# Kernel tuning notes

Hardware: AMD Instinct MI355X
Metric: run time of the kernel (lower is better)

The kernel has to match this reference:

```python
import jax, jax.numpy as jnp
import numpy as np

N, T, D = 2, 8192, 1024          # batch, seq (== maxlen), d_model
G, H, DQ, DV = 1, 16, 64, 64     # gqa groups, heads, d_queries, d_values
S = 16                           # infinite_attention_n_segments
L = T // S                       # segment length
EPS = 1e-05


def setup_inputs() -> dict:
    key = jax.random.key(0)
    ks = jax.random.split(key, 6)
    s = 0.02
    return {
        "x": jax.random.normal(ks[0], (N, T, D), jnp.float32),
        "ln_g": jnp.ones((D,), jnp.float32),
        "ln_b": jnp.zeros((D,), jnp.float32),
        "Wq": jax.random.normal(ks[1], (D, G * H * DQ), jnp.float32) * s,
        "bq": jnp.zeros((G * H * DQ,), jnp.float32),
        "Wk": jax.random.normal(ks[2], (D, H * DQ), jnp.float32) * s,
        "bk": jnp.zeros((H * DQ,), jnp.float32),
        "Wv": jax.random.normal(ks[3], (D, H * DV), jnp.float32) * s,
        "bv": jnp.zeros((H * DV,), jnp.float32),
        "Wo": jax.random.normal(ks[4], (H * DV, D), jnp.float32) * s,
        "bo": jnp.zeros((D,), jnp.float32),
        "beta": jnp.ones((1,), jnp.float32),
    }


def _layernorm(x, g, b):
    mu = jnp.mean(x, axis=-1, keepdims=True)
    var = jnp.mean(jnp.square(x - mu), axis=-1, keepdims=True)
    return (x - mu) * jax.lax.rsqrt(var + EPS) * g + b


def _apply_rotary(t):
    # t: [..., seq, d]; lucidrains rotary-embedding-torch convention (interleaved pairs)
    d, seq = t.shape[-1], t.shape[-2]
    inv = 1.0 / (10000.0 ** (jnp.arange(0, d, 2, dtype=jnp.float32) / d))
    freqs = jnp.arange(seq, dtype=jnp.float32)[:, None] * inv[None, :]  # (seq, d/2)
    freqs = jnp.repeat(freqs, 2, axis=-1)                               # (seq, d)
    cos, sin = jnp.cos(freqs), jnp.sin(freqs)
    x1, x2 = t[..., 0::2], t[..., 1::2]
    rot = jnp.stack([-x2, x1], axis=-1).reshape(t.shape)
    return t * cos + rot * sin


def reference(x, ln_g, ln_b, Wq, bq, Wk, bk, Wv, bv, Wo, bo, beta):
    xn = _layernorm(x, ln_g, ln_b)  # self-attn: same norm for q/k/v
    q = (xn @ Wq + bq).reshape(N, T, G, H, DQ).transpose(0, 2, 3, 1, 4)  # (N,G,H,T,DQ)
    k = (xn @ Wk + bk).reshape(N, T, H, DQ).transpose(0, 2, 1, 3)        # (N,H,T,DQ)
    v = (xn @ Wv + bv).reshape(N, T, H, DV).transpose(0, 2, 1, 3)        # (N,H,T,DV)

    q = _apply_rotary(q)
    k = _apply_rotary(k)

    # segment: (S, N, G, H, L, d) / (S, N, H, L, d)
    qs = jnp.moveaxis(q.reshape(N, G, H, S, L, DQ), 3, 0)
    ks = jnp.moveaxis(k.reshape(N, H, S, L, DQ), 2, 0)
    vs = jnp.moveaxis(v.reshape(N, H, S, L, DV), 2, 0)

    causal = jnp.tril(jnp.ones((L, L), bool))
    scale = 1.0 / (DQ ** 0.5)
    g_beta = jax.nn.sigmoid(beta)[0]

    def step(carry, seg):
        memory, z = carry                     # (N,H,DQ,DV), (N,H,DQ,DQ)
        q_i, k_i, v_i = seg                   # (N,G,H,L,DQ), (N,H,L,DQ), (N,H,L,DV)
        sq = jax.nn.elu(q_i) + 1.0
        sk = jax.nn.elu(k_i) + 1.0
        A_mem = jnp.einsum('nghld,nhde->nghle', sq, memory) / (
            jnp.einsum('nghld,nhde->nghle', sq, z) + 1e-6)
        # note: einsum sums over g (faithful to source); scores (N,H,L,L)
        attn = jnp.einsum('nghld,nhmd->nhlm', q_i, k_i) * scale
        attn = jnp.where(causal, attn, -jnp.inf)
        attn = jax.nn.softmax(attn, axis=-1)
        local = jnp.einsum('nhlm,nhmd->nhld', attn, v_i)
        out = g_beta * A_mem + (1.0 - g_beta) * local[:, None]  # (N,G,H,L,DV)
        memory = memory + jnp.einsum('nhld,nhle->nhde', sk, v_i)          # linear update
        z = z + jnp.sum(sk, axis=-2, keepdims=True)  # (N,H,1,DQ) broadcast (source quirk)
        return (memory, z), out

    mem0 = jnp.zeros((N, H, DQ, DV), jnp.float32)
    z0 = jnp.zeros((N, H, DQ, DQ), jnp.float32)
    _, ys = jax.lax.scan(step, (mem0, z0), (qs, ks, vs))  # ys: (S,N,G,H,L,DV)

    # torch concat along head dim (segment-major) then view(N, t, -1)
    seqs = jnp.transpose(ys, (1, 2, 0, 3, 4, 5)).reshape(N, T, G * H * DV)
    return seqs @ Wo + bo
```

## Files before the change

kernel.cpp:

```cpp
#include <hip/hip_runtime.h>
#include <hip/hip_bf16.h>
#include <math.h>

#define NT 16384
#define DD 1024
#define QKVN 3072

typedef unsigned short u16;
typedef _Float16 half8 __attribute__((ext_vector_type(8)));
typedef float f32x4 __attribute__((ext_vector_type(4)));

#define DEV static __device__ __forceinline__

DEV float h2f(u16 u) { _Float16 h; __builtin_memcpy(&h, &u, 2); return (float)h; }
DEV u16 f2h(float f) { _Float16 h = (_Float16)f; u16 u; __builtin_memcpy(&u, &h, 2); return u; }
DEV f32x4 mfma16(half8 a, half8 b, f32x4 c) {
  return __builtin_amdgcn_mfma_f32_16x16x32_f16(a, b, c, 0, 0, 0);
}
DEV half8 ld8(const u16* p) { return *(const half8*)p; }
DEV float elu1(float x) { return x > 0.f ? x + 1.f : __expf(x); }
DEV void gll16(const void* g, void* l) {
  __builtin_amdgcn_global_load_lds((const __attribute__((address_space(1))) void*)g,
                                   (__attribute__((address_space(3))) void*)l, 16, 0, 0);
}

__global__ __launch_bounds__(256) void prep_w(const float* __restrict__ Wq,
    const float* __restrict__ Wk, const float* __restrict__ Wv,
    const float* __restrict__ Wo, u16* __restrict__ WqkvT, u16* __restrict__ WoT) {
  __shared__ float tile[64][65];
  const int mat = blockIdx.z;
  const float* src = mat == 0 ? Wq : mat == 1 ? Wk : mat == 2 ? Wv : Wo;
  const int d0 = blockIdx.x * 64, c0 = blockIdx.y * 64;
  const int t = threadIdx.x;
#pragma unroll
  for (int i = 0; i < 16; ++i) {
    int rl = (t >> 6) + i * 4;
    tile[rl][t & 63] = src[(size_t)(d0 + rl) * DD + c0 + (t & 63)];
  }
  __syncthreads();
  u16* dst = mat < 3 ? WqkvT + (size_t)mat * DD * DD : WoT;
#pragma unroll
  for (int i = 0; i < 16; ++i) {
    int cl = (t >> 6) + i * 4;
    dst[(size_t)(c0 + cl) * DD + d0 + (t & 63)] = f2h(tile[t & 63][cl]);
  }
}

__global__ void pack_bias(const float* __restrict__ bq, const float* __restrict__ bk,
                          const float* __restrict__ bv, float* __restrict__ bqkv) {
  int i = blockIdx.x * 256 + threadIdx.x;
  if (i < 1024) bqkv[i] = bq[i];
  else if (i < 2048) bqkv[i] = bk[i - 1024];
  else if (i < 3072) bqkv[i] = bv[i - 2048];
}

__global__ __launch_bounds__(256) void rope_table(float* __restrict__ tab) {
  int idx = blockIdx.x * 256 + threadIdx.x;
  int tp = idx >> 5, i = idx & 31;
  double inv = exp(-(double)i * (log(10000.0) / 32.0));
  double ang = (double)tp * inv;
  tab[idx * 2]     = (float)cos(ang);
  tab[idx * 2 + 1] = (float)sin(ang);
}

__global__ __launch_bounds__(256) void lnorm(const float* __restrict__ x,
    const float* __restrict__ g, const float* __restrict__ b, u16* __restrict__ xn) {
  const int row = blockIdx.x, t = threadIdx.x;
  float4 v = ((const float4*)x)[(size_t)row * 256 + t];
  float s = v.x + v.y + v.z + v.w;
  float sq = v.x * v.x + v.y * v.y + v.z * v.z + v.w * v.w;
  for (int o = 32; o; o >>= 1) { s += __shfl_down(s, o); sq += __shfl_down(sq, o); }
  __shared__ float ps[4], pq[4];
  const int w = t >> 6, lane = t & 63;
  if (lane == 0) { ps[w] = s; pq[w] = sq; }
  __syncthreads();
  s = ps[0] + ps[1] + ps[2] + ps[3];
  sq = pq[0] + pq[1] + pq[2] + pq[3];
  float mu = s * (1.f / 1024.f);
  float var = sq * (1.f / 1024.f) - mu * mu;
  float rs = rsqrtf(var + 1e-5f);
  float4 gg = ((const float4*)g)[t], bb = ((const float4*)b)[t];
  float o0 = (v.x - mu) * rs * gg.x + bb.x;
  float o1 = (v.y - mu) * rs * gg.y + bb.y;
  float o2 = (v.z - mu) * rs * gg.z + bb.z;
  float o3 = (v.w - mu) * rs * gg.w + bb.w;
  uint2 u2;
  u2.x = (unsigned)f2h(o0) | ((unsigned)f2h(o1) << 16);
  u2.y = (unsigned)f2h(o2) | ((unsigned)f2h(o3) << 16);
  *(uint2*)&xn[(size_t)row * 1024 + t * 4] = u2;
}

template <bool OUT_F16>
__global__ __launch_bounds__(256) void gemm_bt(const u16* __restrict__ A,
    const u16* __restrict__ BT, const float* __restrict__ bias,
    void* __restrict__ C, int M, int N, int K) {
  __shared__ u16 As[128 * 32];
  __shared__ u16 Bs[128 * 32];
  const int t = threadIdx.x;
  const int lane = t & 63, w = t >> 6;
  const int wr = w >> 1, wc = w & 1;
  const int m0 = blockIdx.x * 128, n0 = blockIdx.y * 128;
  const int srow = w * 16 + (lane >> 2);
  const int schunk = lane & 3;
  int aoff[4], boff[4];
#pragma unroll
  for (int i = 0; i < 4; ++i) {
    int ra = wr * 64 + i * 16 + (lane & 15);
    aoff[i] = ra * 32 + (((lane >> 4) ^ ((ra >> 1) & 3)) * 8);
    int rb = wc * 64 + i * 16 + (lane & 15);
    boff[i] = rb * 32 + (((lane >> 4) ^ ((rb >> 1) & 3)) * 8);
  }
  f32x4 acc[4][4] = {};
  for (int k0 = 0; k0 < K; k0 += 32) {
#pragma unroll
    for (int i = 0; i < 2; ++i) {
      int row = srow + i * 64;
      int gc = (schunk ^ ((row >> 1) & 3)) * 8;
      gll16(&A[(size_t)(m0 + row) * K + k0 + gc], &As[(w * 16 + i * 64) * 32]);
      gll16(&BT[(size_t)(n0 + row) * K + k0 + gc], &Bs[(w * 16 + i * 64) * 32]);
    }
    __syncthreads();
    half8 af[4], bfr[4];
#pragma unroll
    for (int i = 0; i < 4; ++i) {
      af[i]  = ld8(&As[aoff[i]]);
      bfr[i] = ld8(&Bs[boff[i]]);
    }
#pragma unroll
    for (int mi = 0; mi < 4; ++mi)
#pragma unroll
      for (int ni = 0; ni < 4; ++ni)
        acc[mi][ni] = mfma16(af[mi], bfr[ni], acc[mi][ni]);
    __syncthreads();
  }
  const int rg = lane >> 4, cl = lane & 15;
#pragma unroll
  for (int mi = 0; mi < 4; ++mi)
#pragma unroll
    for (int r = 0; r < 4; ++r) {
      size_t row = (size_t)(m0 + wr * 64 + mi * 16 + rg * 4 + r);
#pragma unroll
      for (int ni = 0; ni < 4; ++ni) {
        int col = n0 + wc * 64 + ni * 16 + cl;
        float v = acc[mi][ni][r] + bias[col];
        if (OUT_F16) ((u16*)C)[row * N + col] = f2h(v);
        else ((float*)C)[row * N + col] = v;
      }
    }
}

__global__ __launch_bounds__(256) void rope_apply(u16* __restrict__ qkv,
                                                  const float* __restrict__ tab) {
  const int row = blockIdx.x, t = threadIdx.x;
  const int c = t * 8;
  const int tp = row & 8191;
  const int d0 = c & 63;
  size_t off = (size_t)row * QKVN + c;
  union { uint4 v; u16 s[8]; } q;
  q.v = *(const uint4*)&qkv[off];
  float4 cs0 = *(const float4*)&tab[(tp * 32 + (d0 >> 1)) * 2];
  float4 cs1 = *(const float4*)&tab[(tp * 32 + (d0 >> 1)) * 2 + 4];
  float co[4] = {cs0.x, cs0.z, cs1.x, cs1.z};
  float si[4] = {cs0.y, cs0.w, cs1.y, cs1.w};
#pragma unroll
  for (int j = 0; j < 4; ++j) {
    float x0 = h2f(q.s[2 * j]), x1 = h2f(q.s[2 * j + 1]);
    q.s[2 * j]     = f2h(x0 * co[j] - x1 * si[j]);
    q.s[2 * j + 1] = f2h(x1 * co[j] + x0 * si[j]);
  }
  *(uint4*)&qkv[off] = q.v;
}

__global__ __launch_bounds__(256) void segstats(const u16* __restrict__ qkv,
    float* __restrict__ Mseg, float* __restrict__ Zseg) {
  __shared__ float skL[128][64];
  __shared__ float vL[128][64];
  const int b = blockIdx.x;
  const int seg = b & 15, h = (b >> 4) & 15, n = b >> 8;
  const int t = threadIdx.x;
  const int d = t >> 2, e0 = (t & 3) * 16;
  float acc[16] = {};
  float zacc = 0.f;
  const size_t base = (size_t)(n * 8192 + seg * 512) * QKVN;
  for (int ch = 0; ch < 4; ++ch) {
#pragma unroll
    for (int p = 0; p < 4; ++p) {
      int r = (t >> 3) + 32 * p;
      int cs = (t & 7) * 8;
      size_t ro = base + (size_t)(ch * 128 + r) * QKVN + h * 64 + cs;
      union { uint4 v; u16 s[8]; } kk, vv;
      kk.v = *(const uint4*)&qkv[ro + 1024];
      vv.v = *(const uint4*)&qkv[ro + 2048];
#pragma unroll
      for (int j = 0; j < 8; ++j) {
        skL[r][cs + j] = elu1(h2f(kk.s[j]));
        vL[r][cs + j] = h2f(vv.s[j]);
      }
    }
    __syncthreads();
    for (int l = 0; l < 128; ++l) {
      float s = skL[l][d];
      zacc += s;
      const float4* vr = (const float4*)&vL[l][e0];
      float4 a0 = vr[0], a1 = vr[1], a2 = vr[2], a3 = vr[3];
      acc[0] += s * a0.x;  acc[1] += s * a0.y;  acc[2] += s * a0.z;  acc[3] += s * a0.w;
      acc[4] += s * a1.x;  acc[5] += s * a1.y;  acc[6] += s * a1.z;  acc[7] += s * a1.w;
      acc[8] += s * a2.x;  acc[9] += s * a2.y;  acc[10] += s * a2.z; acc[11] += s * a2.w;
      acc[12] += s * a3.x; acc[13] += s * a3.y; acc[14] += s * a3.z; acc[15] += s * a3.w;
    }
    __syncthreads();
  }
  size_t mb = (size_t)b * 4096 + d * 64 + e0;
  float4 o0 = {acc[0], acc[1], acc[2], acc[3]};
  float4 o1 = {acc[4], acc[5], acc[6], acc[7]};
  float4 o2 = {acc[8], acc[9], acc[10], acc[11]};
  float4 o3 = {acc[12], acc[13], acc[14], acc[15]};
  *(float4*)&Mseg[mb] = o0; *(float4*)&Mseg[mb + 4] = o1;
  *(float4*)&Mseg[mb + 8] = o2; *(float4*)&Mseg[mb + 12] = o3;
  if ((t & 3) == 0) Zseg[(size_t)b * 64 + d] = zacc;
}

__global__ __launch_bounds__(256) void prefix_k(const float* __restrict__ Mseg,
    const float* __restrict__ Zseg, u16* __restrict__ MpT, float* __restrict__ Zpre) {
  const int nh = blockIdx.x;
  const int t = threadIdx.x;
  const int e = t >> 2, d0 = (t & 3) * 16;
  float acc[16] = {};
  for (int s = 0; s < 16; ++s) {
    size_t bb = (size_t)(nh * 16 + s) * 4096;
    union { uint4 v[2]; u16 hh[16]; } o;
#pragma unroll
    for (int j = 0; j < 16; ++j) o.hh[j] = f2h(acc[j]);
    *(uint4*)&MpT[bb + e * 64 + d0] = o.v[0];
    *(uint4*)&MpT[bb + e * 64 + d0 + 8] = o.v[1];
#pragma unroll
    for (int j = 0; j < 16; ++j) acc[j] += Mseg[bb + (size_t)(d0 + j) * 64 + e];
  }
  if (t < 16) {
    float4 zac = {0.f, 0.f, 0.f, 0.f};
    for (int s = 0; s < 16; ++s) {
      size_t idx = (size_t)(nh * 16 + s) * 64 + t * 4;
      *(float4*)&Zpre[idx] = zac;
      float4 z = *(const float4*)&Zseg[idx];
      zac.x += z.x; zac.y += z.y; zac.z += z.z; zac.w += z.w;
    }
  }
}

struct SmemA { u16 Ks[64][72]; u16 VTs[64][72]; u16 Ps[64][72]; };
struct SmemB { u16 sqH[64][72]; u16 MpTs[64][72]; float rowS[64]; };
union SmemU { SmemA a; SmemB b; };

__global__ __launch_bounds__(256, 3) void attn_seg(const u16* __restrict__ qkv,
    const u16* __restrict__ MpT, const float* __restrict__ Zpre,
    const float* __restrict__ beta, u16* __restrict__ ao) {
  __shared__ __align__(16) u16 Qs[64][72];
  __shared__ __align__(16) SmemU U;
  const int b = (blockIdx.x & 7) * 512 + (blockIdx.x >> 3);
  const int qt = b & 7, seg = (b >> 3) & 15, h = (b >> 7) & 15, n = b >> 11;
  const int t = threadIdx.x, lane = t & 63, w = t >> 6;

  const size_t qbase = (size_t)(n * 8192 + seg * 512 + qt * 64) * QKVN + h * 64;
#pragma unroll
  for (int p = 0; p < 2; ++p) {
    int r = p * 32 + (t >> 3), cs = (t & 7) * 8;
    *(uint4*)&Qs[r][cs] = *(const uint4*)&qkv[qbase + (size_t)r * QKVN + cs];
  }

  const int r0 = t >> 3;
  const int cs = (t & 7) * 8;
  const int vcol1 = (((w) ^ (t & 7)) << 3) | (r0 & 7);
  const int vcol2 = (((w + 4) ^ (t & 7)) << 3) | (r0 & 7);
  const size_t kbase = (size_t)(n * 8192 + seg * 512) * QKVN + h * 64 + cs;

  uint4 kk0, kk1, vv0, vv1;
  {
    size_t ro = kbase + (size_t)r0 * QKVN;
    kk0 = *(const uint4*)&qkv[ro + 1024];
    vv0 = *(const uint4*)&qkv[ro + 2048];
    kk1 = *(const uint4*)&qkv[ro + 32 * QKVN + 1024];
    vv1 = *(const uint4*)&qkv[ro + 32 * QKVN + 2048];
  }
  __syncthreads();
  half8 aq0 = ld8(&Qs[w * 16 + (lane & 15)][(lane >> 4) * 8]);
  half8 aq1 = ld8(&Qs[w * 16 + (lane & 15)][32 + (lane >> 4) * 8]);

  float mrow[4], lrow[4];
  f32x4 oacc[4] = {};
#pragma unroll
  for (int r = 0; r < 4; ++r) { mrow[r] = -INFINITY; lrow[r] = 0.f; }

  for (int mt = 0; mt <= qt; ++mt) {
    *(uint4*)&U.a.Ks[r0][cs] = kk0;
    *(uint4*)&U.a.Ks[r0 + 32][cs] = kk1;
    union { uint4 v; u16 s[8]; } u0, u1;
    u0.v = vv0; u1.v = vv1;
#pragma unroll
    for (int j = 0; j < 8; ++j) {
      U.a.VTs[cs + j][vcol1] = u0.s[j];
      U.a.VTs[cs + j][vcol2] = u1.s[j];
    }
    if (mt < qt) {
      size_t ro = kbase + (size_t)((mt + 1) * 64 + r0) * QKVN;
      kk0 = *(const uint4*)&qkv[ro + 1024];
      vv0 = *(const uint4*)&qkv[ro + 2048];
      kk1 = *(const uint4*)&qkv[ro + 32 * QKVN + 1024];
      vv1 = *(const uint4*)&qkv[ro + 32 * QKVN + 2048];
    }
    __syncthreads();

    f32x4 s[4] = {};
#pragma unroll
    for (int ni = 0; ni < 4; ++ni) {
      half8 b0 = ld8(&U.a.Ks[ni * 16 + (lane & 15)][(lane >> 4) * 8]);
      half8 b1 = ld8(&U.a.Ks[ni * 16 + (lane & 15)][32 + (lane >> 4) * 8]);
      s[ni] = mfma16(aq0, b0, s[ni]);
      s[ni] = mfma16(aq1, b1, s[ni]);
    }
    float pm[4];
#pragma unroll
    for (int r = 0; r < 4; ++r) {
      int ql = qt * 64 + w * 16 + (lane >> 4) * 4 + r;
      float mx = -INFINITY;
#pragma unroll
      for (int ni = 0; ni < 4; ++ni) {
        float v = s[ni][r] * 0.125f;
        if (mt == qt) { int ml = mt * 64 + ni * 16 + (lane & 15); if (ml > ql) v = -INFINITY; }
        s[ni][r] = v; mx = fmaxf(mx, v);
      }
      pm[r] = mx;
    }
#pragma unroll
    for (int o = 1; o < 16; o <<= 1)
#pragma unroll
      for (int r = 0; r < 4; ++r) pm[r] = fmaxf(pm[r], __shfl_xor(pm[r], o, 16));
    float fac[4], rs[4];
#pragma unroll
    for (int r = 0; r < 4; ++r) {
      float mn = fmaxf(mrow[r], pm[r]);
      fac[r] = __expf(mrow[r] - mn);
      mrow[r] = mn;
      float a = 0.f;
#pragma unroll
      for (int ni = 0; ni < 4; ++ni) { float p = __expf(s[ni][r] - mn); s[ni][r] = p; a += p; }
      rs[r] = a;
    }
#pragma unroll
    for (int o = 1; o < 16; o <<= 1)
#pragma unroll
      for (int r = 0; r < 4; ++r) rs[r] += __shfl_xor(rs[r], o, 16);
#pragma unroll
    for (int r = 0; r < 4; ++r) {
      lrow[r] = lrow[r] * fac[r] + rs[r];
#pragma unroll
      for (int ei = 0; ei < 4; ++ei) oacc[ei][r] *= fac[r];
    }
#pragma unroll
    for (int ni = 0; ni < 4; ++ni)
#pragma unroll
      for (int r = 0; r < 4; ++r)
        U.a.Ps[w * 16 + (lane >> 4) * 4 + r][ni * 16 + (lane & 15)] = f2h(s[ni][r]);
#pragma unroll
    for (int ks = 0; ks < 2; ++ks) {
      half8 ap = ld8(&U.a.Ps[w * 16 + (lane & 15)][ks * 32 + (lane >> 4) * 8]);
#pragma unroll
      for (int ei = 0; ei < 4; ++ei) {
        int erow = ei * 16 + (lane & 15);
        int ccol = (((ks * 4 + (lane >> 4)) ^ (ei * 2 + ((lane & 15) >> 3))) << 3);
        half8 bv = ld8(&U.a.VTs[erow][ccol]);
        oacc[ei] = mfma16(ap, bv, oacc[ei]);
      }
    }
    __syncthreads();
  }

  {
    const int q = t >> 2, c0 = (t & 3) * 16;
    union { uint2 v; u16 s[4]; } qa;
    float partial = 0.f;
    union { uint4 v; u16 hh[8]; } o;
#pragma unroll
    for (int half = 0; half < 2; ++half) {
#pragma unroll
      for (int jj = 0; jj < 2; ++jj) {
        qa.v = *(const uint2*)&Qs[q][c0 + half * 8 + jj * 4];
#pragma unroll
        for (int k4 = 0; k4 < 4; ++k4) {
          float sv = elu1(h2f(qa.s[k4]));
          partial += sv;
          o.hh[jj * 4 + k4] = f2h(sv);
        }
      }
      *(uint4*)&U.b.sqH[q][c0 + half * 8] = o.v;
    }
    partial += __shfl_xor(partial, 1);
    partial += __shfl_xor(partial, 2);
    if ((t & 3) == 0) U.b.rowS[q] = partial;
  }
  const size_t mpb = (size_t)((n * 16 + h) * 16 + seg) * 4096;
#pragma unroll
  for (int p = 0; p < 2; ++p) {
    int e = p * 32 + (t >> 3), c = (t & 7) * 8;
    *(uint4*)&U.b.MpTs[e][c] = *(const uint4*)&MpT[mpb + e * 64 + c];
  }
  __syncthreads();

  f32x4 num[4] = {};
#pragma unroll
  for (int ks = 0; ks < 2; ++ks) {
    half8 asq = ld8(&U.b.sqH[w * 16 + (lane & 15)][ks * 32 + (lane >> 4) * 8]);
#pragma unroll
    for (int ni = 0; ni < 4; ++ni) {
      half8 bmp = ld8(&U.b.MpTs[ni * 16 + (lane & 15)][ks * 32 + (lane >> 4) * 8]);
      num[ni] = mfma16(asq, bmp, num[ni]);
    }
  }

  const float gb = 1.f / (1.f + __expf(-beta[0]));
  const size_t zb = (size_t)((n * 16 + h) * 16 + seg) * 64;
  const int g = lane >> 4;
  float rsv[4];
#pragma unroll
  for (int r = 0; r < 4; ++r) rsv[r] = U.b.rowS[w * 16 + g * 4 + r];
  const size_t orow = ((size_t)(n * 8192 + seg * 512 + h * 32 + qt * 4 + w)) * 1024;
#pragma unroll
  for (int ni = 0; ni < 4; ++ni) {
    float z = Zpre[zb + ni * 16 + (lane & 15)];
#pragma unroll
    for (int r = 0; r < 4; ++r) {
      float am = num[ni][r] / (rsv[r] * z + 1e-6f);
      float loc = oacc[ni][r] / lrow[r];
      float val = gb * am + (1.f - gb) * loc;
      ao[orow + (size_t)(g * 4 + r) * 64 + ni * 16 + (lane & 15)] = f2h(val);
    }
  }
}

extern "C" void kernel_launch(void* const* d_in, const int* in_sizes, int n_in,
                              void* d_out, int out_size, void* d_ws, size_t ws_size,
                              hipStream_t stream) {
  const float* x    = (const float*)d_in[0];
  const float* ln_g = (const float*)d_in[1];
  const float* ln_b = (const float*)d_in[2];
  const float* Wq   = (const float*)d_in[3];
  const float* bq   = (const float*)d_in[4];
  const float* Wk   = (const float*)d_in[5];
  const float* bk   = (const float*)d_in[6];
  const float* Wv   = (const float*)d_in[7];
  const float* bv   = (const float*)d_in[8];
  const float* Wo   = (const float*)d_in[9];
  const float* bo   = (const float*)d_in[10];
  const float* beta = (const float*)d_in[11];
  float* out = (float*)d_out;

  char* w = (char*)d_ws;
  u16*   xn    = (u16*)(w + 0);
  u16*   qkv   = (u16*)(w + 33554432ull);
  u16*   WqkvT = (u16*)(w + 134217728ull);
  u16*   WoT   = (u16*)(w + 140509184ull);
  float* bqkv  = (float*)(w + 142606336ull);
  float* tab   = (float*)(w + 142618624ull);
  float* Mseg  = (float*)(w + 144715776ull);
  float* Zseg  = (float*)(w + 153104384ull);
  u16*   MpT   = (u16*)(w + 153235456ull);
  float* Zpre  = (float*)(w + 161624064ull);
  u16*   ao    = (u16*)(w + 161755136ull);

  prep_w<<<dim3(16, 16, 4), 256, 0, stream>>>(Wq, Wk, Wv, Wo, WqkvT, WoT);
  pack_bias<<<12, 256, 0, stream>>>(bq, bk, bv, bqkv);
  rope_table<<<1024, 256, 0, stream>>>(tab);
  lnorm<<<16384, 256, 0, stream>>>(x, ln_g, ln_b, xn);
  gemm_bt<true><<<dim3(128, 24), 256, 0, stream>>>(xn, WqkvT, bqkv, (void*)qkv, NT, QKVN, DD);
  rope_apply<<<16384, 256, 0, stream>>>(qkv, tab);
  segstats<<<512, 256, 0, stream>>>(qkv, Mseg, Zseg);
  prefix_k<<<32, 256, 0, stream>>>(Mseg, Zseg, MpT, Zpre);
  attn_seg<<<4096, 256, 0, stream>>>(qkv, MpT, Zpre, beta, ao);
  gemm_bt<false><<<dim3(128, 8), 256, 0, stream>>>(ao, WoT, bo, (void*)out, NT, DD, DD);
}
```

Measured before the change: 524.9 us.

## Use 256x256 double-buffered GEMM and transpose segment stats for coalesced prefix

Replaces the 128x128 single-buffered GEMM with a 256x256-tile, 512-thread kernel. The new kernel double-buffers K-chunks in 128KB of dynamic LDS, interleaves global-to-LDS staging with MFMA phases, raises wave priority during MFMA and swizzles block IDs for L2 locality. Segstats now transposes its memory stats through LDS so prefix_k reads contiguous float4 and spreads over 128 blocks instead of 32. The large LDS footprint limits occupancy, and the hand-written vmcnt waits must match the load counts exactly.

Result: faster. 489.7 us (-6.7%).

```diff
diff --git a/kernel.cpp b/kernel.cpp
--- a/kernel.cpp
+++ b/kernel.cpp
@@ -91,57 +91,125 @@
 }
 
 template <bool OUT_F16>
-__global__ __launch_bounds__(256) void gemm_bt(const u16* __restrict__ A,
+__global__ __launch_bounds__(512, 2) void gemm256(const u16* __restrict__ A,
     const u16* __restrict__ BT, const float* __restrict__ bias,
-    void* __restrict__ C, int M, int N, int K) {
-  __shared__ u16 As[128 * 32];
-  __shared__ u16 Bs[128 * 32];
-  const int t = threadIdx.x;
-  const int lane = t & 63, w = t >> 6;
-  const int wr = w >> 1, wc = w & 1;
-  const int m0 = blockIdx.x * 128, n0 = blockIdx.y * 128;
-  const int srow = w * 16 + (lane >> 2);
-  const int schunk = lane & 3;
-  int aoff[4], boff[4];
-#pragma unroll
-  for (int i = 0; i < 4; ++i) {
-    int ra = wr * 64 + i * 16 + (lane & 15);
-    aoff[i] = ra * 32 + (((lane >> 4) ^ ((ra >> 1) & 3)) * 8);
-    int rb = wc * 64 + i * 16 + (lane & 15);
-    boff[i] = rb * 32 + (((lane >> 4) ^ ((rb >> 1) & 3)) * 8);
-  }
-  f32x4 acc[4][4] = {};
-  for (int k0 = 0; k0 < K; k0 += 32) {
-#pragma unroll
-    for (int i = 0; i < 2; ++i) {
-      int row = srow + i * 64;
-      int gc = (schunk ^ ((row >> 1) & 3)) * 8;
-      gll16(&A[(size_t)(m0 + row) * K + k0 + gc], &As[(w * 16 + i * 64) * 32]);
-      gll16(&BT[(size_t)(n0 + row) * K + k0 + gc], &Bs[(w * 16 + i * 64) * 32]);
-    }
-    __syncthreads();
-    half8 af[4], bfr[4];
-#pragma unroll
-    for (int i = 0; i < 4; ++i) {
-      af[i]  = ld8(&As[aoff[i]]);
-      bfr[i] = ld8(&Bs[boff[i]]);
-    }
+    void* __restrict__ C, int M, int N, int K, int gx) {
+  extern __shared__ __align__(16) u16 lds[];
+  u16* As = lds;
+  u16* Bs = lds + 32768;
+  const int t = threadIdx.x, lane = t & 63, w = t >> 6;
+  const int wm = w >> 2, wn = w & 3;
+  const int nwg = gridDim.x, bid = blockIdx.x;
+  const int swz = (bid & 7) * (nwg >> 3) + (bid >> 3);
+  const int bx = swz % gx, by = swz / gx;
+  const int m0 = bx * 256, n0 = by * 256;
+  const int NTK = K >> 6;
+  const u16* Ab = A + (size_t)m0 * K;
+  const u16* Bb = BT + (size_t)n0 * K;
+
+  int aoff[8], boff[4];
+#pragma unroll
+  for (int mi = 0; mi < 8; ++mi) {
+    int ra = wm * 128 + mi * 16 + (lane & 15);
+    aoff[mi] = ra * 32 + (((lane >> 4) ^ ((ra >> 1) & 3)) * 8);
+  }
+#pragma unroll
+  for (int ni = 0; ni < 4; ++ni) {
+    int rb = wn * 64 + ni * 16 + (lane & 15);
+    boff[ni] = rb * 32 + (((lane >> 4) ^ ((rb >> 1) & 3)) * 8);
+  }
+  const int r1 = w * 16 + (lane >> 2);
+  const int r2 = 128 + r1;
+  const int c1 = ((lane & 3) ^ ((r1 >> 1) & 3)) * 8;
+  const int c2 = ((lane & 3) ^ ((r2 >> 1) & 3)) * 8;
+  const int l1 = (w * 16) * 32;
+  const int l2 = (128 + w * 16) * 32;
+
+#define STAGE(Gb, Lp, kc)                                          \
+  { gll16(&Gb[(size_t)r1 * K + (kc) + c1], (Lp) + l1);             \
+    gll16(&Gb[(size_t)r2 * K + (kc) + c2], (Lp) + l2); }
+
+  f32x4 acc[8][4] = {};
+  STAGE(Ab, As, 0);
+  STAGE(Bb, Bs, 0);
+  STAGE(Ab, As + 8192, 32);
+  STAGE(Bb, Bs + 8192, 32);
+
+  half8 af[4], bf[4];
+  for (int kt = 0; kt < NTK; ++kt) {
+    const int cur = kt & 1;
+    u16* Ac = As + cur * 16384;
+    u16* Bc = Bs + cur * 16384;
+    u16* An = As + (cur ^ 1) * 16384;
+    u16* Bn = Bs + (cur ^ 1) * 16384;
+    const int kn = (kt + 1) * 64;
+    const bool more = (kt + 1 < NTK);
+    asm volatile("s_waitcnt vmcnt(4)" ::: "memory");
+    if (more) STAGE(Ab, An, kn);
+    __builtin_amdgcn_s_barrier();
+#pragma unroll
+    for (int i = 0; i < 4; ++i) af[i] = ld8(Ac + aoff[i]);
+#pragma unroll
+    for (int i = 0; i < 4; ++i) bf[i] = ld8(Bc + boff[i]);
+    __builtin_amdgcn_s_setprio(1);
 #pragma unroll
     for (int mi = 0; mi < 4; ++mi)
 #pragma unroll
       for (int ni = 0; ni < 4; ++ni)
-        acc[mi][ni] = mfma16(af[mi], bfr[ni], acc[mi][ni]);
-    __syncthreads();
-  }
+        acc[mi][ni] = mfma16(af[mi], bf[ni], acc[mi][ni]);
+    __builtin_amdgcn_s_setprio(0);
+    __builtin_amdgcn_s_barrier();
+    if (more) STAGE(Bb, Bn, kn);
+    __builtin_amdgcn_s_barrier();
+#pragma unroll
+    for (int i = 0; i < 4; ++i) af[i] = ld8(Ac + aoff[4 + i]);
+    __builtin_amdgcn_s_setprio(1);
+#pragma unroll
+    for (int mi = 0; mi < 4; ++mi)
+#pragma unroll
+      for (int ni = 0; ni < 4; ++ni)
+        acc[4 + mi][ni] = mfma16(af[mi], bf[ni], acc[4 + mi][ni]);
+    __builtin_amdgcn_s_setprio(0);
+    __builtin_amdgcn_s_barrier();
+    if (more) { asm volatile("s_waitcnt vmcnt(4)" ::: "memory"); }
+    else      { asm volatile("s_waitcnt vmcnt(0)" ::: "memory"); }
+    if (more) STAGE(Ab, An + 8192, kn + 32);
+    __builtin_amdgcn_s_barrier();
+#pragma unroll
+    for (int i = 0; i < 4; ++i) af[i] = ld8(Ac + 8192 + aoff[i]);
+#pragma unroll
+    for (int i = 0; i < 4; ++i) bf[i] = ld8(Bc + 8192 + boff[i]);
+    __builtin_amdgcn_s_setprio(1);
+#pragma unroll
+    for (int mi = 0; mi < 4; ++mi)
+#pragma unroll
+      for (int ni = 0; ni < 4; ++ni)
+        acc[mi][ni] = mfma16(af[mi], bf[ni], acc[mi][ni]);
+    __builtin_amdgcn_s_setprio(0);
+    __builtin_amdgcn_s_barrier();
+    if (more) STAGE(Bb, Bn + 8192, kn + 32);
+    __builtin_amdgcn_s_barrier();
+#pragma unroll
+    for (int i = 0; i < 4; ++i) af[i] = ld8(Ac + 8192 + aoff[4 + i]);
+    __builtin_amdgcn_s_setprio(1);
+#pragma unroll
+    for (int mi = 0; mi < 4; ++mi)
+#pragma unroll
+      for (int ni = 0; ni < 4; ++ni)
+        acc[4 + mi][ni] = mfma16(af[mi], bf[ni], acc[4 + mi][ni]);
+    __builtin_amdgcn_s_setprio(0);
+    __builtin_amdgcn_s_barrier();
+  }
+#undef STAGE
   const int rg = lane >> 4, cl = lane & 15;
 #pragma unroll
-  for (int mi = 0; mi < 4; ++mi)
+  for (int mi = 0; mi < 8; ++mi)
 #pragma unroll
     for (int r = 0; r < 4; ++r) {
-      size_t row = (size_t)(m0 + wr * 64 + mi * 16 + rg * 4 + r);
+      size_t row = (size_t)(m0 + wm * 128 + mi * 16 + rg * 4 + r);
 #pragma unroll
       for (int ni = 0; ni < 4; ++ni) {
-        int col = n0 + wc * 64 + ni * 16 + cl;
+        int col = n0 + wn * 64 + ni * 16 + cl;
         float v = acc[mi][ni][r] + bias[col];
         if (OUT_F16) ((u16*)C)[row * N + col] = f2h(v);
         else ((float*)C)[row * N + col] = v;
@@ -172,7 +240,7 @@
 }
 
 __global__ __launch_bounds__(256) void segstats(const u16* __restrict__ qkv,
-    float* __restrict__ Mseg, float* __restrict__ Zseg) {
+    float* __restrict__ MsegT, float* __restrict__ Zseg) {
   __shared__ float skL[128][64];
   __shared__ float vL[128][64];
   const int b = blockIdx.x;
@@ -210,33 +278,39 @@
     }
     __syncthreads();
   }
-  size_t mb = (size_t)b * 4096 + d * 64 + e0;
-  float4 o0 = {acc[0], acc[1], acc[2], acc[3]};
-  float4 o1 = {acc[4], acc[5], acc[6], acc[7]};
-  float4 o2 = {acc[8], acc[9], acc[10], acc[11]};
-  float4 o3 = {acc[12], acc[13], acc[14], acc[15]};
-  *(float4*)&Mseg[mb] = o0; *(float4*)&Mseg[mb + 4] = o1;
-  *(float4*)&Mseg[mb + 8] = o2; *(float4*)&Mseg[mb + 12] = o3;
   if ((t & 3) == 0) Zseg[(size_t)b * 64 + d] = zacc;
-}
-
-__global__ __launch_bounds__(256) void prefix_k(const float* __restrict__ Mseg,
+  float* tr = &skL[0][0];
+#pragma unroll
+  for (int j = 0; j < 16; ++j) tr[d * 65 + e0 + j] = acc[j];
+  __syncthreads();
+  const int e2 = t >> 2, d02 = (t & 3) * 16;
+  float ov[16];
+#pragma unroll
+  for (int j = 0; j < 16; ++j) ov[j] = tr[(d02 + j) * 65 + e2];
+  size_t mb = (size_t)b * 4096 + e2 * 64 + d02;
+#pragma unroll
+  for (int j4 = 0; j4 < 4; ++j4) {
+    float4 o = {ov[j4 * 4], ov[j4 * 4 + 1], ov[j4 * 4 + 2], ov[j4 * 4 + 3]};
+    *(float4*)&MsegT[mb + j4 * 4] = o;
+  }
+}
+
+__global__ __launch_bounds__(256) void prefix_k(const float* __restrict__ MsegT,
     const float* __restrict__ Zseg, u16* __restrict__ MpT, float* __restrict__ Zpre) {
-  const int nh = blockIdx.x;
+  const int nh = blockIdx.x >> 2, eg = blockIdx.x & 3;
   const int t = threadIdx.x;
-  const int e = t >> 2, d0 = (t & 3) * 16;
-  float acc[16] = {};
+  const int e = eg * 16 + (t >> 4), d4 = (t & 15) * 4;
+  float4 acc = {0.f, 0.f, 0.f, 0.f};
   for (int s = 0; s < 16; ++s) {
-    size_t bb = (size_t)(nh * 16 + s) * 4096;
-    union { uint4 v[2]; u16 hh[16]; } o;
-#pragma unroll
-    for (int j = 0; j < 16; ++j) o.hh[j] = f2h(acc[j]);
-    *(uint4*)&MpT[bb + e * 64 + d0] = o.v[0];
-    *(uint4*)&MpT[bb + e * 64 + d0 + 8] = o.v[1];
-#pragma unroll
-    for (int j = 0; j < 16; ++j) acc[j] += Mseg[bb + (size_t)(d0 + j) * 64 + e];
-  }
-  if (t < 16) {
+    size_t idx = (size_t)(nh * 16 + s) * 4096 + e * 64 + d4;
+    union { uint2 v; u16 hh[4]; } o;
+    o.hh[0] = f2h(acc.x); o.hh[1] = f2h(acc.y);
+    o.hh[2] = f2h(acc.z); o.hh[3] = f2h(acc.w);
+    *(uint2*)&MpT[idx] = o.v;
+    float4 m = *(const float4*)&MsegT[idx];
+    acc.x += m.x; acc.y += m.y; acc.z += m.z; acc.w += m.w;
+  }
+  if (eg == 0 && t < 16) {
     float4 zac = {0.f, 0.f, 0.f, 0.f};
     for (int s = 0; s < 16; ++s) {
       size_t idx = (size_t)(nh * 16 + s) * 64 + t * 4;
@@ -460,20 +534,27 @@
   u16*   WoT   = (u16*)(w + 140509184ull);
   float* bqkv  = (float*)(w + 142606336ull);
   float* tab   = (float*)(w + 142618624ull);
-  float* Mseg  = (float*)(w + 144715776ull);
+  float* MsegT = (float*)(w + 144715776ull);
   float* Zseg  = (float*)(w + 153104384ull);
   u16*   MpT   = (u16*)(w + 153235456ull);
   float* Zpre  = (float*)(w + 161624064ull);
   u16*   ao    = (u16*)(w + 161755136ull);
 
+  hipFuncSetAttribute((const void*)&gemm256<true>,
+                      hipFuncAttributeMaxDynamicSharedMemorySize, 131072);
+  hipFuncSetAttribute((const void*)&gemm256<false>,
+                      hipFuncAttributeMaxDynamicSharedMemorySize, 131072);
+
   prep_w<<<dim3(16, 16, 4), 256, 0, stream>>>(Wq, Wk, Wv, Wo, WqkvT, WoT);
   pack_bias<<<12, 256, 0, stream>>>(bq, bk, bv, bqkv);
   rope_table<<<1024, 256, 0, stream>>>(tab);
   lnorm<<<16384, 256, 0, stream>>>(x, ln_g, ln_b, xn);
-  gemm_bt<true><<<dim3(128, 24), 256, 0, stream>>>(xn, WqkvT, bqkv, (void*)qkv, NT, QKVN, DD);
+  gemm256<true><<<768, 512, 131072, stream>>>(xn, WqkvT, bqkv, (void*)qkv,
+                                              NT, QKVN, DD, 64);
   rope_apply<<<16384, 256, 0, stream>>>(qkv, tab);
-  segstats<<<512, 256, 0, stream>>>(qkv, Mseg, Zseg);
-  prefix_k<<<32, 256, 0, stream>>>(Mseg, Zseg, MpT, Zpre);
+  segstats<<<512, 256, 0, stream>>>(qkv, MsegT, Zseg);
+  prefix_k<<<128, 256, 0, stream>>>(MsegT, Zseg, MpT, Zpre);
   attn_seg<<<4096, 256, 0, stream>>>(qkv, MpT, Zpre, beta, ao);
-  gemm_bt<false><<<dim3(128, 8), 256, 0, stream>>>(ao, WoT, bo, (void*)out, NT, DD, DD);
-}
+  gemm256<false><<<256, 512, 131072, stream>>>(ao, WoT, bo, (void*)out,
+                                               NT, DD, DD, 64);
+}
```
